# Kernel optimization log

Hardware: AMD Instinct MI355X
Metric: run time of the kernel (lower is better)

## Reference

```python
import jax, jax.numpy as jnp
import numpy as np

C, D = 256, 8192        # n_components, n_curves (x_shape_0, x_shape_1)
Q = 32                  # truncation_q
HID = 4096              # hidden_dim
Y0, Y1 = 512, 2048      # y_shape_0, y_shape_1
WN_H = 64               # weight-network hidden width


def setup_inputs() -> dict:
    key = jax.random.key(0)
    ks = jax.random.split(key, 11)
    def s(k, shape, scale):
        return jax.random.normal(k, shape, dtype=jnp.float32) * scale
    return {
        "X": s(ks[0], (C, D), 1.0),
        # WeightNetwork: scalar lag -> scalar weight, 2-layer MLP with GELU
        "wn_w1": s(ks[1], (1, WN_H), 0.5),
        "wn_b1": s(ks[2], (WN_H,), 0.1),
        "wn_w2": s(ks[3], (WN_H, 1), 1.0 / np.sqrt(WN_H)),
        "wn_b2": s(ks[4], (1,), 0.1),
        # fc1: Linear(2*D, HID); fc2: Linear(HID, Y1); stored as (in, out)
        "fc1_w": s(ks[5], (2 * D, HID), 1.0 / np.sqrt(2 * D)),
        "fc1_b": s(ks[6], (HID,), 0.01),
        "fc2_w": s(ks[7], (HID, Y1), 1.0 / np.sqrt(HID)),
        "fc2_b": s(ks[8], (Y1,), 0.01),
        "proj": s(ks[9], (Y0, C), 1.0),
        "trunc_q": Q,
    }


def _gelu(x):
    # torch nn.GELU default = exact erf form
    return jax.nn.gelu(x, approximate=False)


def _lr_cov(X, wn_w1, wn_b1, wn_w2, wn_b2, q):
    """Batched equivalent of the per-pair ccovf loop (adjusted, demeaned).

    ccovf(x_i, x_j)[k] = sum_t (x_i[t+k]-mu_i)(x_j[t]-mu_j) / (n-k)
    cov[i,j] = sum_{k=-q..q} w[k] * gamma_{|k|}[i,j]  (negative lags reuse
    gamma_k of the (i,j) ordering, exactly as in the torch code).
    """
    n = X.shape[1]
    Xo = X - jnp.mean(X, axis=1, keepdims=True)
    # kernel weights from the weight network over lags -q..q
    lags = jnp.arange(-q, q + 1, dtype=jnp.float32)
    h = _gelu(lags[:, None] @ wn_w1 + wn_b1)
    w = (h @ wn_w2 + wn_b2)[:, 0]                      # (2q+1,)
    # lag-0 term
    cov = (w[q] / n) * (Xo @ Xo.T)
    # lags 1..q: gamma_k = Xo[:, k:] @ Xo[:, :n-k].T / (n-k)
    for k in range(1, q + 1):
        g = (Xo[:, k:] @ Xo[:, : n - k].T) / (n - k)   # (C, C)
        cov = cov + (w[q - k] + w[q + k]) * g
    return cov


def reference(X, wn_w1, wn_b1, wn_w2, wn_b2, fc1_w, fc1_b, fc2_w, fc2_b, proj, trunc_q):
    cov = _lr_cov(X, wn_w1, wn_b1, wn_w2, wn_b2, trunc_q)   # (C, C)
    cov_interaction = cov @ X                               # (C, D)
    combined = jnp.concatenate([X, cov_interaction], axis=1)  # (C, 2D)
    out = _gelu(combined @ fc1_w + fc1_b)                   # (C, HID)
    out = _gelu(out @ fc2_w + fc2_b)                        # (C, Y1)
    return proj @ out                                       # (Y0, Y1)
```

## Files before the change

kernel.cpp:

```cpp
#include <hip/hip_runtime.h>
#include <math.h>

typedef unsigned short u16;
typedef unsigned int   u32;

typedef __bf16 bf16x8 __attribute__((ext_vector_type(8)));
typedef float  f32x4  __attribute__((ext_vector_type(4)));

#define C_DIM 256
#define D_DIM 8192
#define HIDD  4096
#define Y1D   2048

__device__ __forceinline__ u16 f2bf(float f) {
    union { float f; u32 u; } v; v.f = f;
    u32 r = v.u + 0x7fffu + ((v.u >> 16) & 1u);
    return (u16)(r >> 16);
}
__device__ __forceinline__ float geluf(float x) {
    return 0.5f * x * (1.0f + erff(x * 0.70710678118654752f));
}
__device__ __forceinline__ int swz(int row, int kg) {
    return row * 64 + (((kg) ^ ((row >> 1) & 3)) << 4);
}
__device__ __forceinline__ int xsw(int t) {
    int ch = t >> 2;
    return (((ch ^ ((ch >> 3) & 7))) << 2) | (t & 3);
}
__device__ __forceinline__ void gload16(const void* g, void* l) {
    __builtin_amdgcn_global_load_lds(
        (const __attribute__((address_space(1))) void*)g,
        (__attribute__((address_space(3))) void*)l, 16, 0, 0);
}

__global__ __launch_bounds__(256) void filterk(const float* __restrict__ X,
                                               const float* __restrict__ w1,
                                               const float* __restrict__ b1,
                                               const float* __restrict__ w2,
                                               const float* __restrict__ b2,
                                               u16* __restrict__ Zb,
                                               u16* __restrict__ Xob,
                                               u16* __restrict__ Xb) {
    __shared__ float Xl[8240];
    __shared__ float wl[65];
    __shared__ float cl[40];
    __shared__ float red[4];
    int i = blockIdx.x, tid = threadIdx.x;
    int lane = tid & 63, wv = tid >> 6;
    const float* row = X + (size_t)i * D_DIM;
    float s = 0.f;
    #pragma unroll
    for (int q = 0; q < 8; ++q) {
        int t = tid * 32 + q * 4;
        float4 v = *(const float4*)(row + t);
        s += v.x + v.y + v.z + v.w;
        *(float4*)(Xl + xsw(t)) = v;
    }
    float w1l = w1[lane], b1l = b1[lane], w2l = w2[lane], b2l = b2[0];
    for (int li = wv; li < 65; li += 4) {
        float lag = (float)(li - 32);
        float h = geluf(lag * w1l + b1l);
        float p = h * w2l;
        #pragma unroll
        for (int off = 32; off; off >>= 1) p += __shfl_xor(p, off);
        if (lane == 0) wl[li] = p + b2l;
    }
    #pragma unroll
    for (int off = 32; off; off >>= 1) s += __shfl_xor(s, off);
    if (lane == 0) red[wv] = s;
    __syncthreads();
    if (tid <= 32) {
        cl[tid] = (tid == 0) ? wl[32] / (float)D_DIM
                             : (wl[32 - tid] + wl[32 + tid]) / ((float)D_DIM - (float)tid);
    }
    if (tid == 33) {
        float ssum = wl[32] / (float)D_DIM;
        for (int k = 1; k <= 32; ++k) ssum += (wl[32 - k] + wl[32 + k]) / ((float)D_DIM - (float)k);
        cl[33] = ssum;
    }
    float mu = (red[0] + red[1] + red[2] + red[3]) * (1.f / (float)D_DIM);
    if (tid < 10) {
        float4 mv = make_float4(mu, mu, mu, mu);
        *(float4*)(Xl + xsw(D_DIM + tid * 4)) = mv;
    }
    __syncthreads();
    float csum = cl[33];
    #pragma unroll
    for (int ch = 0; ch < 8; ++ch) {
        int t4 = tid * 32 + ch * 4;
        float w[40] __attribute__((aligned(16)));
        #pragma unroll
        for (int g = 0; g < 10; ++g)
            *(float4*)(w + g * 4) = *(const float4*)(Xl + xsw(t4 + g * 4));
        u16 zb[4], xo[4], xb[4];
        #pragma unroll
        for (int j = 0; j < 4; ++j) {
            float a = 0.f;
            #pragma unroll
            for (int k = 0; k < 33; ++k) a = fmaf(cl[k], w[j + k], a);
            zb[j] = f2bf(a - mu * csum);
            xo[j] = f2bf(w[j] - mu);
            xb[j] = f2bf(w[j]);
        }
        uint2 zp, op, bp;
        zp.x = (u32)zb[0] | ((u32)zb[1] << 16); zp.y = (u32)zb[2] | ((u32)zb[3] << 16);
        op.x = (u32)xo[0] | ((u32)xo[1] << 16); op.y = (u32)xo[2] | ((u32)xo[3] << 16);
        bp.x = (u32)xb[0] | ((u32)xb[1] << 16); bp.y = (u32)xb[2] | ((u32)xb[3] << 16);
        *(uint2*)(Zb  + (size_t)i * D_DIM + t4) = zp;
        *(uint2*)(Xob + (size_t)i * D_DIM + t4) = op;
        *(uint2*)(Xb  + (size_t)i * D_DIM + t4) = bp;
    }
}

template<int MODE, int ASRC, int BSRC, int BN, int KS>
__global__ __launch_bounds__(512) void gemm_u(
    const void* __restrict__ Av, int lda,
    const void* __restrict__ Bv, int ldb,
    int N, int sliceLen, int nHalf, long long bHalfOff,
    const float* __restrict__ Vadd, const float* __restrict__ bias,
    float* __restrict__ outF, u16* __restrict__ outB,
    int ldc, int partStride)
{
    constexpr int NI = BN / 32;
    __shared__ u16 Alds[2][256 * 32];
    __shared__ u16 Blds[2][BN * 32];
    const int tid = threadIdx.x;
    const int bid = blockIdx.x;
    const int ks  = bid % KS;
    const int nb0 = (bid / KS) * BN;
    const int mt  = blockIdx.y;
    const int k0base = ks * sliceLen;
    const int ksteps = sliceLen >> 5;
    const int lane = tid & 63, wid = tid >> 6;
    const int wm = wid >> 1, wn = wid & 1;
    const int l15 = lane & 15, kg = lane >> 4;

    const int inH2 = (nb0 >= nHalf) ? 1 : 0;
    const int nbB  = nb0 - (inH2 ? nHalf : 0);

    const u16* gA0 = nullptr; const u16* gA1 = nullptr;
    {
        int r0 = wid * 32 + (lane >> 2);
        int r1 = r0 + 16;
        int c0 = (lane & 3) ^ ((r0 >> 1) & 3);
        int c1 = (lane & 3) ^ ((r1 >> 1) & 3);
        gA0 = (const u16*)Av + (size_t)(mt * 256 + r0) * lda + k0base + c0 * 8;
        gA1 = (const u16*)Av + (size_t)(mt * 256 + r1) * lda + k0base + c1 * 8;
    }
    const int sArow = tid >> 1, sAe = (tid & 1) * 16;
    const float* ApF = (const float*)Av + (size_t)(mt * 256 + sArow) * lda + sAe + k0base;
    const int aw0 = swz(sArow, sAe >> 3);
    const int aw1 = swz(sArow, (sAe >> 3) + 1);
    float4 fa0, fa1, fa2, fa3;

    const int n2 = (tid & 31) * 2;
    const int k4 = ((tid >> 5) & 7) * 4;
    const float* BpF = (const float*)Bv + (inH2 ? (size_t)bHalfOff : 0)
                     + (size_t)(k0base + k4) * ldb + nbB + n2;
    const int bwc0 = swz(n2,     k4 >> 3) + (k4 & 4) * 2;
    const int bwc1 = swz(n2 + 1, k4 >> 3) + (k4 & 4) * 2;
    float2 Lb0, Lb1, Lb2, Lb3;
    const u16* gB0 = nullptr;
    if constexpr (BSRC == 1) {
        int tr = wid * 16 + (lane >> 2);
        int c  = (lane & 3) ^ ((tr >> 1) & 3);
        gB0 = (const u16*)Bv + (size_t)(nb0 + tr) * ldb + k0base + c * 8;
    }
    const int sBk = tid >> 4, sBn2 = (tid & 15) * 2;
    const u16* BpH = (const u16*)Bv + (size_t)(k0base + sBk) * ldb + nbB + sBn2;
    const int bh0 = swz(sBn2,     sBk >> 3) + (sBk & 7) * 2;
    const int bh1 = swz(sBn2 + 1, sBk >> 3) + (sBk & 7) * 2;
    u32 bhv = 0;

    int aoff[4], boff[NI];
    #pragma unroll
    for (int mi = 0; mi < 4; ++mi) { int r = wm * 64 + mi * 16 + l15; aoff[mi] = swz(r, kg); }
    #pragma unroll
    for (int ni = 0; ni < NI; ++ni) { int r = wn * (BN / 2) + ni * 16 + l15; boff[ni] = swz(r, kg); }

    auto stageGL = [&](int kt, int pb) {
        if constexpr (ASRC == 0) {
            char* ab = (char*)&Alds[pb][0] + wid * 2048;
            gload16(gA0 + (kt << 5), ab);
            gload16(gA1 + (kt << 5), ab + 1024);
        }
        if constexpr (BSRC == 1) {
            if (wid < BN / 16) {
                char* bb = (char*)&Blds[pb][0] + wid * 1024;
                gload16(gB0 + (kt << 5), bb);
            }
        }
    };
    auto loadA = [&](int kt) {
        const float* ap = ApF + (kt << 5);
        fa0 = *(const float4*)(ap);     fa1 = *(const float4*)(ap + 4);
        fa2 = *(const float4*)(ap + 8); fa3 = *(const float4*)(ap + 12);
    };
    auto writeA = [&](int pb) {
        char* AB = (char*)&Alds[pb][0];
        int4 w0, w1;
        w0.x = (int)((u32)f2bf(fa0.x) | ((u32)f2bf(fa0.y) << 16));
        w0.y = (int)((u32)f2bf(fa0.z) | ((u32)f2bf(fa0.w) << 16));
        w0.z = (int)((u32)f2bf(fa1.x) | ((u32)f2bf(fa1.y) << 16));
        w0.w = (int)((u32)f2bf(fa1.z) | ((u32)f2bf(fa1.w) << 16));
        w1.x = (int)((u32)f2bf(fa2.x) | ((u32)f2bf(fa2.y) << 16));
        w1.y = (int)((u32)f2bf(fa2.z) | ((u32)f2bf(fa2.w) << 16));
        w1.z = (int)((u32)f2bf(fa3.x) | ((u32)f2bf(fa3.y) << 16));
        w1.w = (int)((u32)f2bf(fa3.z) | ((u32)f2bf(fa3.w) << 16));
        *(int4*)(AB + aw0) = w0;
        *(int4*)(AB + aw1) = w1;
    };
    auto loadB = [&](int kt) {
        if constexpr (BSRC == 0) {
            if (tid < 256) {
                const float* bp = BpF + (size_t)(kt << 5) * ldb;
                Lb0 = *(const float2*)(bp);
                Lb1 = *(const float2*)(bp + ldb);
                Lb2 = *(const float2*)(bp + 2 * ldb);
                Lb3 = *(const float2*)(bp + 3 * ldb);
            }
        } else if constexpr (BSRC == 2) {
            bhv = *(const u32*)(BpH + (size_t)(kt << 5) * ldb);
        }
    };
    auto writeB = [&](int pb) {
        char* BB = (char*)&Blds[pb][0];
        if constexpr (BSRC == 0) {
            if (tid < 256) {
                uint2 p0, p1;
                p0.x = (u32)f2bf(Lb0.x) | ((u32)f2bf(Lb1.x) << 16);
                p0.y = (u32)f2bf(Lb2.x) | ((u32)f2bf(Lb3.x) << 16);
                p1.x = (u32)f2bf(Lb0.y) | ((u32)f2bf(Lb1.y) << 16);
                p1.y = (u32)f2bf(Lb2.y) | ((u32)f2bf(Lb3.y) << 16);
                *(uint2*)(BB + bwc0) = p0;
                *(uint2*)(BB + bwc1) = p1;
            }
        } else if constexpr (BSRC == 2) {
            *(u16*)(BB + bh0) = (u16)(bhv & 0xffffu);
            *(u16*)(BB + bh1) = (u16)(bhv >> 16);
        }
    };

    f32x4 acc[4][NI];
    #pragma unroll
    for (int mi = 0; mi < 4; ++mi)
        #pragma unroll
        for (int ni = 0; ni < NI; ++ni) { f32x4 zz = {0.f, 0.f, 0.f, 0.f}; acc[mi][ni] = zz; }

    auto mfmaStep = [&](int pb) {
        const char* AB = (const char*)&Alds[pb][0];
        const char* BB = (const char*)&Blds[pb][0];
        bf16x8 af[4], bfr[NI];
        #pragma unroll
        for (int mi = 0; mi < 4; ++mi) af[mi] = *(const bf16x8*)(AB + aoff[mi]);
        #pragma unroll
        for (int ni = 0; ni < NI; ++ni) bfr[ni] = *(const bf16x8*)(BB + boff[ni]);
        #pragma unroll
        for (int mi = 0; mi < 4; ++mi)
            #pragma unroll
            for (int ni = 0; ni < NI; ++ni)
                acc[mi][ni] = __builtin_amdgcn_mfma_f32_16x16x32_bf16(af[mi], bfr[ni], acc[mi][ni], 0, 0, 0);
    };

    stageGL(0, 0);
    if constexpr (ASRC == 1) { loadA(0); writeA(0); loadA(1); }
    if constexpr (BSRC == 0 || BSRC == 2) { loadB(0); writeB(0); loadB(1); }
    __syncthreads();
    for (int kt = 0; kt < ksteps; ++kt) {
        const int pb = kt & 1;
        if (kt + 1 < ksteps) {
            stageGL(kt + 1, pb ^ 1);
            if constexpr (ASRC == 1) writeA(pb ^ 1);
            if constexpr (BSRC == 0 || BSRC == 2) writeB(pb ^ 1);
        }
        if (kt + 2 < ksteps) {
            if constexpr (ASRC == 1) loadA(kt + 2);
            if constexpr (BSRC == 0 || BSRC == 2) loadB(kt + 2);
        }
        mfmaStep(pb);
        __syncthreads();
    }

    const int rq = lane >> 4;
    #pragma unroll
    for (int mi = 0; mi < 4; ++mi)
        #pragma unroll
        for (int ni = 0; ni < NI; ++ni)
            #pragma unroll
            for (int r = 0; r < 4; ++r) {
                int m = wm * 64 + mi * 16 + rq * 4 + r;
                int n = nb0 + wn * (BN / 2) + ni * 16 + l15;
                float v = acc[mi][ni][r];
                if (MODE == 0)
                    outB[(size_t)ks * partStride + (size_t)m * N + n] = f2bf(v);
                else if (MODE == 2)
                    outF[(size_t)(mt * 256 + m) * ldc + n] = v;
                else {
                    float h = geluf(v + Vadd[(size_t)m * N + n] + bias[n]);
                    outB[(size_t)m * ldc + n] = f2bf(h);
                }
            }
}

__global__ __launch_bounds__(256) void reduce_cov(const u16* __restrict__ parts,
                                                  u16* __restrict__ out) {
    int i8 = (blockIdx.x * 256 + threadIdx.x) * 8;
    float s[8] = {};
    #pragma unroll
    for (int sl = 0; sl < 32; ++sl) {
        uint4 v = *(const uint4*)(parts + (size_t)sl * 65536 + i8);
        u32 w[4] = {v.x, v.y, v.z, v.w};
        #pragma unroll
        for (int j = 0; j < 4; ++j) {
            union { u32 u; float f; } lo, hi;
            lo.u = (w[j] & 0xffffu) << 16; hi.u = w[j] & 0xffff0000u;
            s[2 * j] += lo.f; s[2 * j + 1] += hi.f;
        }
    }
    uint4 pk;
    pk.x = (u32)f2bf(s[0]) | ((u32)f2bf(s[1]) << 16);
    pk.y = (u32)f2bf(s[2]) | ((u32)f2bf(s[3]) << 16);
    pk.z = (u32)f2bf(s[4]) | ((u32)f2bf(s[5]) << 16);
    pk.w = (u32)f2bf(s[6]) | ((u32)f2bf(s[7]) << 16);
    *(uint4*)(out + i8) = pk;
}

__global__ __launch_bounds__(256) void reduce_vu(const u16* __restrict__ parts,
                                                 float* __restrict__ V,
                                                 u16* __restrict__ U) {
    int i8 = (blockIdx.x * 256 + threadIdx.x) * 8;
    int m = i8 >> 13, n = i8 & 8191;
    float s[8] = {};
    #pragma unroll
    for (int sl = 0; sl < 8; ++sl) {
        uint4 v = *(const uint4*)(parts + (size_t)sl * (256 * 8192) + i8);
        u32 w[4] = {v.x, v.y, v.z, v.w};
        #pragma unroll
        for (int j = 0; j < 4; ++j) {
            union { u32 u; float f; } lo, hi;
            lo.u = (w[j] & 0xffffu) << 16; hi.u = w[j] & 0xffff0000u;
            s[2 * j] += lo.f; s[2 * j + 1] += hi.f;
        }
    }
    if (n < 4096) {
        float* vp = V + (size_t)m * 4096 + n;
        *(float4*)(vp)     = make_float4(s[0], s[1], s[2], s[3]);
        *(float4*)(vp + 4) = make_float4(s[4], s[5], s[6], s[7]);
    } else {
        uint4 pk;
        pk.x = (u32)f2bf(s[0]) | ((u32)f2bf(s[1]) << 16);
        pk.y = (u32)f2bf(s[2]) | ((u32)f2bf(s[3]) << 16);
        pk.z = (u32)f2bf(s[4]) | ((u32)f2bf(s[5]) << 16);
        pk.w = (u32)f2bf(s[6]) | ((u32)f2bf(s[7]) << 16);
        *(uint4*)(U + (size_t)m * 4096 + (n - 4096)) = pk;
    }
}

__global__ __launch_bounds__(256) void reduce_fc16(const u16* __restrict__ parts,
                                                   const float* __restrict__ bias,
                                                   float* __restrict__ outF) {
    int i8 = (blockIdx.x * 256 + threadIdx.x) * 8;
    int col = i8 & (Y1D - 1);
    float s[8] = {};
    #pragma unroll
    for (int sl = 0; sl < 16; ++sl) {
        uint4 v = *(const uint4*)(parts + (size_t)sl * (256 * Y1D) + i8);
        u32 w[4] = {v.x, v.y, v.z, v.w};
        #pragma unroll
        for (int j = 0; j < 4; ++j) {
            union { u32 u; float f; } lo, hi;
            lo.u = (w[j] & 0xffffu) << 16; hi.u = w[j] & 0xffff0000u;
            s[2 * j] += lo.f; s[2 * j + 1] += hi.f;
        }
    }
    float4 b0 = *(const float4*)(bias + col);
    float4 b1 = *(const float4*)(bias + col + 4);
    s[0] = geluf(s[0] + b0.x); s[1] = geluf(s[1] + b0.y);
    s[2] = geluf(s[2] + b0.z); s[3] = geluf(s[3] + b0.w);
    s[4] = geluf(s[4] + b1.x); s[5] = geluf(s[5] + b1.y);
    s[6] = geluf(s[6] + b1.z); s[7] = geluf(s[7] + b1.w);
    *(float4*)(outF + i8)     = make_float4(s[0], s[1], s[2], s[3]);
    *(float4*)(outF + i8 + 4) = make_float4(s[4], s[5], s[6], s[7]);
}

extern "C" void kernel_launch(void* const* d_in, const int* in_sizes, int n_in,
                              void* d_out, int out_size, void* d_ws, size_t ws_size,
                              hipStream_t stream) {
    const float* X     = (const float*)d_in[0];
    const float* wn_w1 = (const float*)d_in[1];
    const float* wn_b1 = (const float*)d_in[2];
    const float* wn_w2 = (const float*)d_in[3];
    const float* wn_b2 = (const float*)d_in[4];
    const float* fc1_w = (const float*)d_in[5];
    const float* fc1_b = (const float*)d_in[6];
    const float* fc2_w = (const float*)d_in[7];
    const float* fc2_b = (const float*)d_in[8];
    const float* proj  = (const float*)d_in[9];

    char* ws = (char*)d_ws;
    size_t off = 0;
    auto alloc = [&](size_t bytes) { size_t o = off; off += (bytes + 255) & ~(size_t)255; return o; };
    u16*   Zb    = (u16*)  (ws + alloc((size_t)C_DIM * D_DIM * 2));
    u16*   Xob   = (u16*)  (ws + alloc((size_t)C_DIM * D_DIM * 2));
    u16*   Xb    = (u16*)  (ws + alloc((size_t)C_DIM * D_DIM * 2));
    u16*   covp  = (u16*)  (ws + alloc((size_t)32 * 65536 * 2));
    u16*   covbf = (u16*)  (ws + alloc((size_t)65536 * 2));
    u16*   p1b   = (u16*)  (ws + alloc((size_t)8 * C_DIM * D_DIM * 2));
    float* Vf    = (float*)(ws + alloc((size_t)C_DIM * HIDD * 4));
    u16*   Ubf   = (u16*)  (ws + alloc((size_t)C_DIM * HIDD * 2));
    u16*   hbf   = (u16*)  (ws + alloc((size_t)C_DIM * HIDD * 2));
    u16*   p2b   = (u16*)  (ws + alloc((size_t)16 * C_DIM * Y1D * 2));
    float* of32  = (float*)(ws + alloc((size_t)C_DIM * Y1D * 4));

    filterk<<<C_DIM, 256, 0, stream>>>(X, wn_w1, wn_b1, wn_w2, wn_b2, Zb, Xob, Xb);
    gemm_u<0, 0, 1, 64, 32><<<128, 512, 0, stream>>>(Zb, D_DIM, Xob, D_DIM,
        C_DIM, D_DIM / 32, C_DIM, 0, nullptr, nullptr, nullptr, covp, 0, 65536);
    reduce_cov<<<32, 256, 0, stream>>>(covp, covbf);
    gemm_u<0, 0, 0, 64, 8><<<(2 * HIDD / 64) * 8, 512, 0, stream>>>(Xb, D_DIM, fc1_w, HIDD,
        2 * HIDD, D_DIM / 8, HIDD, (long long)D_DIM * HIDD, nullptr, nullptr,
        nullptr, p1b, 0, C_DIM * 2 * HIDD);
    reduce_vu<<<1024, 256, 0, stream>>>(p1b, Vf, Ubf);
    gemm_u<3, 0, 2, 32, 1><<<HIDD / 32, 512, 0, stream>>>(covbf, C_DIM, Ubf, HIDD,
        HIDD, C_DIM, HIDD, 0, Vf, fc1_b, nullptr, hbf, HIDD, 0);
    gemm_u<0, 0, 0, 64, 16><<<(Y1D / 64) * 16, 512, 0, stream>>>(hbf, HIDD, fc2_w, Y1D,
        Y1D, HIDD / 16, Y1D, 0, nullptr, nullptr, nullptr, p2b, 0, C_DIM * Y1D);
    reduce_fc16<<<C_DIM * Y1D / 8 / 256, 256, 0, stream>>>(p2b, fc2_b, of32);
    gemm_u<2, 1, 0, 64, 1><<<dim3(Y1D / 64, 2), 512, 0, stream>>>(proj, C_DIM, of32, Y1D,
        Y1D, C_DIM, Y1D, 0, nullptr, nullptr, (float*)d_out, nullptr, Y1D, 0);
}
```

Measured before the change: 200.2 us.

## Add 4-stage pipelined split-K GEMM with M split for fc1 and fc2

Adds a new gemm_p kernel used for the fc1 and fc2 weight GEMMs. It tiles M into 128-row halves across blockIdx.y, doubling the block count, and uses a 4-deep LDS ring buffer with three stages in flight via direct global-to-LDS loads. The fp32 weights are converted to bf16 fragments from LDS inside the loop. The aim is more latency hiding and more parallelism for these memory-bound weight streams. In exchange, each fc weight tile is now read twice (once per M half), and each step does extra scalar LDS reads and conversion work.

```diff
diff --git a/kernel.cpp b/kernel.cpp
--- a/kernel.cpp
+++ b/kernel.cpp
@@ -110,6 +110,101 @@
         *(uint2*)(Xob + (size_t)i * D_DIM + t4) = op;
         *(uint2*)(Xb  + (size_t)i * D_DIM + t4) = bp;
     }
+}
+
+template<int KS>
+__global__ __launch_bounds__(512) void gemm_p(
+    const u16* __restrict__ A, int lda,
+    const float* __restrict__ B, int ldb,
+    int N, int sliceLen, int nHalf, long long bHalfOff,
+    u16* __restrict__ outB, int partStride)
+{
+    __shared__ u16  A4[4][128 * 32];
+    __shared__ float B4[4][32 * 64];
+    const int tid = threadIdx.x;
+    const int bid = blockIdx.x;
+    const int ks  = bid % KS;
+    const int nb0 = (bid / KS) * 64;
+    const int mt  = blockIdx.y;
+    const int k0base = ks * sliceLen;
+    const int ksteps = sliceLen >> 5;
+    const int lane = tid & 63, wid = tid >> 6;
+    const int wm = wid >> 1, wn = wid & 1;
+    const int l15 = lane & 15, kg = lane >> 4;
+
+    const int inH2 = (nb0 >= nHalf) ? 1 : 0;
+    const int nbB  = nb0 - (inH2 ? nHalf : 0);
+
+    const int arow = tid >> 2;
+    const int achk = (tid & 3) ^ ((arow >> 1) & 3);
+    const u16* gA = A + (size_t)(mt * 128 + arow) * lda + k0base + achk * 8;
+    const int bk = tid >> 4, bng = tid & 15;
+    const float* gB = B + (inH2 ? (size_t)bHalfOff : 0)
+                    + (size_t)(k0base + bk) * ldb + nbB + bng * 4;
+    int aoff[2];
+    #pragma unroll
+    for (int mi = 0; mi < 2; ++mi) aoff[mi] = swz(wm * 32 + mi * 16 + l15, kg);
+    int bnidx[2];
+    #pragma unroll
+    for (int ni = 0; ni < 2; ++ni) bnidx[ni] = wn * 32 + ni * 16 + l15;
+
+    f32x4 acc[2][2];
+    #pragma unroll
+    for (int mi = 0; mi < 2; ++mi)
+        #pragma unroll
+        for (int ni = 0; ni < 2; ++ni) { f32x4 zz = {0.f, 0.f, 0.f, 0.f}; acc[mi][ni] = zz; }
+
+    auto stage = [&](int kt, int buf) {
+        gload16(gA + (kt << 5), (char*)&A4[buf][0] + wid * 1024);
+        gload16(gB + (size_t)(kt << 5) * ldb, (char*)&B4[buf][0] + wid * 1024);
+    };
+
+    stage(0, 0); stage(1, 1); stage(2, 2);
+    for (int kt = 0; kt < ksteps; ++kt) {
+        const int st = (kt + 3 < ksteps) ? kt + 3 : ksteps - 1;
+        stage(st, (kt + 3) & 3);
+        asm volatile("s_waitcnt vmcnt(6)" ::: "memory");
+        __builtin_amdgcn_sched_barrier(0);
+        __builtin_amdgcn_s_barrier();
+        __builtin_amdgcn_sched_barrier(0);
+        const int buf = kt & 3;
+        const char*  AB = (const char*)&A4[buf][0];
+        const float* BB = &B4[buf][0];
+        bf16x8 af[2], bfrag[2];
+        #pragma unroll
+        for (int mi = 0; mi < 2; ++mi) af[mi] = *(const bf16x8*)(AB + aoff[mi]);
+        #pragma unroll
+        for (int ni = 0; ni < 2; ++ni) {
+            union { u32 u[4]; bf16x8 v; } pk;
+            #pragma unroll
+            for (int j = 0; j < 4; ++j) {
+                float lo = BB[(kg * 8 + 2 * j)     * 64 + bnidx[ni]];
+                float hi = BB[(kg * 8 + 2 * j + 1) * 64 + bnidx[ni]];
+                pk.u[j] = (u32)f2bf(lo) | ((u32)f2bf(hi) << 16);
+            }
+            bfrag[ni] = pk.v;
+        }
+        #pragma unroll
+        for (int mi = 0; mi < 2; ++mi)
+            #pragma unroll
+            for (int ni = 0; ni < 2; ++ni)
+                acc[mi][ni] = __builtin_amdgcn_mfma_f32_16x16x32_bf16(af[mi], bfrag[ni], acc[mi][ni], 0, 0, 0);
+        __builtin_amdgcn_sched_barrier(0);
+        __builtin_amdgcn_s_barrier();
+        __builtin_amdgcn_sched_barrier(0);
+    }
+
+    const int rq = lane >> 4;
+    #pragma unroll
+    for (int mi = 0; mi < 2; ++mi)
+        #pragma unroll
+        for (int ni = 0; ni < 2; ++ni)
+            #pragma unroll
+            for (int r = 0; r < 4; ++r) {
+                int m = mt * 128 + wm * 32 + mi * 16 + rq * 4 + r;
+                int n = nb0 + wn * 32 + ni * 16 + l15;
+                outB[(size_t)ks * partStride + (size_t)m * N + n] = f2bf(acc[mi][ni][r]);
+            }
 }
 
 template<int MODE, int ASRC, int BSRC, int BN, int KS>
@@ -416,14 +511,13 @@
     gemm_u<0, 0, 1, 64, 32><<<128, 512, 0, stream>>>(Zb, D_DIM, Xob, D_DIM,
         C_DIM, D_DIM / 32, C_DIM, 0, nullptr, nullptr, nullptr, covp, 0, 65536);
     reduce_cov<<<32, 256, 0, stream>>>(covp, covbf);
-    gemm_u<0, 0, 0, 64, 8><<<(2 * HIDD / 64) * 8, 512, 0, stream>>>(Xb, D_DIM, fc1_w, HIDD,
-        2 * HIDD, D_DIM / 8, HIDD, (long long)D_DIM * HIDD, nullptr, nullptr,
-        nullptr, p1b, 0, C_DIM * 2 * HIDD);
+    gemm_p<8><<<dim3((2 * HIDD / 64) * 8, 2), 512, 0, stream>>>(Xb, D_DIM, fc1_w, HIDD,
+        2 * HIDD, D_DIM / 8, HIDD, (long long)D_DIM * HIDD, p1b, C_DIM * 2 * HIDD);
     reduce_vu<<<1024, 256, 0, stream>>>(p1b, Vf, Ubf);
     gemm_u<3, 0, 2, 32, 1><<<HIDD / 32, 512, 0, stream>>>(covbf, C_DIM, Ubf, HIDD,
         HIDD, C_DIM, HIDD, 0, Vf, fc1_b, nullptr, hbf, HIDD, 0);
-    gemm_u<0, 0, 0, 64, 16><<<(Y1D / 64) * 16, 512, 0, stream>>>(hbf, HIDD, fc2_w, Y1D,
-        Y1D, HIDD / 16, Y1D, 0, nullptr, nullptr, nullptr, p2b, 0, C_DIM * Y1D);
+    gemm_p<16><<<dim3((Y1D / 64) * 16, 2), 512, 0, stream>>>(hbf, HIDD, fc2_w, Y1D,
+        Y1D, HIDD / 16, Y1D, 0, p2b, C_DIM * Y1D);
     reduce_fc16<<<C_DIM * Y1D / 8 / 256, 256, 0, stream>>>(p2b, fc2_b, of32);
     gemm_u<2, 1, 0, 64, 1><<<dim3(Y1D / 64, 2), 512, 0, stream>>>(proj, C_DIM, of32, Y1D,
         Y1D, C_DIM, Y1D, 0, nullptr, nullptr, (float*)d_out, nullptr, Y1D, 0);
```

After: 267.7 us. +33.7%, slower.

## Replace LDS-staged fc1/fc2 GEMMs with direct-load register MFMA kernel

Applied to the files above, without the earlier changes.

Adds a gemm_s kernel that skips shared-memory staging. Each wave loads its fp32 B column slice straight from global memory, converts it to bf16 in registers, and reads A bf16 fragments directly from global or L2, with 16 accumulator tiles covering all 256 rows. Both the fc1 and fc2 split-K GEMMs use it, which removes LDS round trips and barriers on these weight-streaming, bandwidth-bound GEMMs. The cost is many more uncoalesced global reads of A, which is re-read by every wave, and strided 4-byte B loads that may use bandwidth less efficiently.

```diff
diff --git a/kernel.cpp b/kernel.cpp
--- a/kernel.cpp
+++ b/kernel.cpp
@@ -110,6 +110,61 @@
         *(uint2*)(Xob + (size_t)i * D_DIM + t4) = op;
         *(uint2*)(Xb  + (size_t)i * D_DIM + t4) = bp;
     }
+}
+
+template<int KS, int LDA>
+__global__ __launch_bounds__(256) void gemm_s(
+    const u16* __restrict__ A,
+    const float* __restrict__ B,
+    int ldb, int N, int sliceLen, int nHalf, long long bHalfOff,
+    u16* __restrict__ outB, int partStride)
+{
+    const int tid = threadIdx.x;
+    const int bid = blockIdx.x;
+    const int ks  = bid % KS;
+    const int nb0 = (bid / KS) * 64;
+    const int lane = tid & 63, wid = tid >> 6;
+    const int nb = nb0 + wid * 16;
+    const int l15 = lane & 15, kg = lane >> 4;
+    const int k0base = ks * sliceLen;
+    const int ksteps = sliceLen >> 5;
+
+    const int inH2 = (nb >= nHalf) ? 1 : 0;
+    const int nbB  = nb - (inH2 ? nHalf : 0);
+
+    const u16* Ab = A + (size_t)l15 * LDA + k0base + kg * 8;
+    const float* Bb = B + (inH2 ? (size_t)bHalfOff : 0)
+                    + (size_t)(k0base + kg * 8) * ldb + nbB + l15;
+
+    f32x4 acc[16];
+    #pragma unroll
+    for (int mi = 0; mi < 16; ++mi) { f32x4 zz = {0.f, 0.f, 0.f, 0.f}; acc[mi] = zz; }
+
+    for (int kt = 0; kt < ksteps; ++kt) {
+        const float* bp = Bb + (size_t)(kt << 5) * ldb;
+        float b[8];
+        #pragma unroll
+        for (int j = 0; j < 8; ++j) b[j] = bp[(size_t)j * ldb];
+        union { u32 u[4]; bf16x8 v; } bfr;
+        #pragma unroll
+        for (int j = 0; j < 4; ++j)
+            asm("v_cvt_pk_bf16_f32 %0, %1, %2"
+                : "=v"(bfr.u[j]) : "v"(b[2 * j]), "v"(b[2 * j + 1]));
+        #pragma unroll
+        for (int mi = 0; mi < 16; ++mi) {
+            bf16x8 af = *(const bf16x8*)(Ab + (size_t)mi * 16 * LDA + (kt << 5));
+            acc[mi] = __builtin_amdgcn_mfma_f32_16x16x32_bf16(af, bfr.v, acc[mi], 0, 0, 0);
+        }
+    }
+
+    const int rq = lane >> 4;
+    #pragma unroll
+    for (int mi = 0; mi < 16; ++mi)
+        #pragma unroll
+        for (int r = 0; r < 4; ++r) {
+            int m = mi * 16 + rq * 4 + r;
+            outB[(size_t)ks * partStride + (size_t)m * N + nb + l15] = f2bf(acc[mi][r]);
+        }
 }
 
 template<int MODE, int ASRC, int BSRC, int BN, int KS>
@@ -416,14 +471,13 @@
     gemm_u<0, 0, 1, 64, 32><<<128, 512, 0, stream>>>(Zb, D_DIM, Xob, D_DIM,
         C_DIM, D_DIM / 32, C_DIM, 0, nullptr, nullptr, nullptr, covp, 0, 65536);
     reduce_cov<<<32, 256, 0, stream>>>(covp, covbf);
-    gemm_u<0, 0, 0, 64, 8><<<(2 * HIDD / 64) * 8, 512, 0, stream>>>(Xb, D_DIM, fc1_w, HIDD,
-        2 * HIDD, D_DIM / 8, HIDD, (long long)D_DIM * HIDD, nullptr, nullptr,
-        nullptr, p1b, 0, C_DIM * 2 * HIDD);
+    gemm_s<8, D_DIM><<<(2 * HIDD / 64) * 8, 256, 0, stream>>>(Xb, fc1_w, HIDD,
+        2 * HIDD, D_DIM / 8, HIDD, (long long)D_DIM * HIDD, p1b, C_DIM * 2 * HIDD);
     reduce_vu<<<1024, 256, 0, stream>>>(p1b, Vf, Ubf);
     gemm_u<3, 0, 2, 32, 1><<<HIDD / 32, 512, 0, stream>>>(covbf, C_DIM, Ubf, HIDD,
         HIDD, C_DIM, HIDD, 0, Vf, fc1_b, nullptr, hbf, HIDD, 0);
-    gemm_u<0, 0, 0, 64, 16><<<(Y1D / 64) * 16, 512, 0, stream>>>(hbf, HIDD, fc2_w, Y1D,
-        Y1D, HIDD / 16, Y1D, 0, nullptr, nullptr, nullptr, p2b, 0, C_DIM * Y1D);
+    gemm_s<16, HIDD><<<(Y1D / 64) * 16, 256, 0, stream>>>(hbf, fc2_w, Y1D,
+        Y1D, HIDD / 16, 1 << 30, 0, p2b, C_DIM * Y1D);
     reduce_fc16<<<C_DIM * Y1D / 8 / 256, 256, 0, stream>>>(p2b, fc2_b, of32);
     gemm_u<2, 1, 0, 64, 1><<<dim3(Y1D / 64, 2), 512, 0, stream>>>(proj, C_DIM, of32, Y1D,
         Y1D, C_DIM, Y1D, 0, nullptr, nullptr, (float*)d_out, nullptr, Y1D, 0);
```

After: 562.1 us. 2.81x slower.
